# Kernel tuning notes

Hardware: AMD Instinct MI355X
Metric: run time of the kernel (lower is better)

Reference implementation:

```python
import jax, jax.numpy as jnp
import numpy as np

SIGMA = 0.5          # init kwarg sigma
PATCH = 5            # init kwarg patch_size
TILE = 32            # init kwarg patch_distance (tile side)
H_PARAM = (PATCH // 2) ** 0.5  # self.h = sqrt(patch_size//2)


def _nlm(tiles, sigma, p, Hp):
    # tiles: [b, c, h, w] -- faithful jax port of nlm()
    b, c, h, w = tiles.shape
    pad = p // 2
    padded = jnp.pad(tiles, ((0, 0), (0, 0), (pad, pad), (pad, pad)), mode='edge')  # replicate pad
    # unfold: all p*p shifted views -> [b, c, p*p, h, w] (channel-major then patch index,
    # matching torch unfold + unflatten(1, (c, p*p)))
    pats = jnp.stack([padded[:, :, i:i + h, j:j + w]
                      for i in range(p) for j in range(p)], axis=2)
    center = p * p // 2
    keep = np.array([k for k in range(p * p) if k != center])
    N = h * w
    d = c * (p * p - 1)
    yN = pats[:, :, keep].reshape(b, d, N).transpose(0, 2, 1)  # [b, N, d]
    # pairwise euclidean distance (cdist)
    sq = jnp.sum(yN * yN, axis=-1)  # [b, N]
    d2 = sq[:, :, None] + sq[:, None, :] - 2.0 * jnp.einsum('bnd,bmd->bnm', yN, yN)
    dist = jnp.sqrt(jnp.maximum(d2, 0.0))  # [b, N, N]
    density = jnp.exp(-dist / (2.0 * Hp ** 2 * sigma ** 2))
    # diag set to +inf in dist -> density diag = 0
    density = density * (1.0 - jnp.eye(N, dtype=density.dtype))
    weight = density / jnp.sum(density, axis=-1, keepdims=True)  # [b, N, N]
    y = tiles.reshape(b, c, N)  # [b, c, N]
    mmse = jnp.einsum('bnm,bcm->bcn', weight, y)  # weighted sum of pixel values
    return mmse.reshape(b, c, h, w)


def reference(image):
    # Tile image into non-overlapping TILE x TILE tiles, run nlm batched, fold back.
    b, c, h, w = image.shape
    T = TILE
    nh, nw = h // T, w // T
    tiles = image.reshape(b, c, nh, T, nw, T).transpose(0, 2, 4, 1, 3, 5)
    tiles = tiles.reshape(b * nh * nw, c, T, T)
    out = _nlm(tiles, SIGMA, PATCH, H_PARAM)
    out = out.reshape(b, nh, nw, c, T, T).transpose(0, 3, 1, 4, 2, 5)
    return out.reshape(b, c, h, w)


def setup_inputs() -> dict:
    key = jax.random.key(0)
    image = jax.random.uniform(key, (1, 3, 320, 320), dtype=jnp.float32)
    return {"image": image}
```

## Files before the change

kernel.cpp:

```cpp
#include <hip/hip_runtime.h>
#include <math.h>

#define TS   32
#define PT   36
#define NPIX 1024
#define DF   72
#define KP   96
#define IMH  320
#define IMW  320
#define NTW  10
#define NTILE 100

#define F_UNITS_PER_TILE 12288
#define FHI_BYTES (NTILE * F_UNITS_PER_TILE * 16)
#define SQ_OFF    (2 * FHI_BYTES)

#define K2LOG2E 2.0813689810056077f

typedef __attribute__((ext_vector_type(8))) short bf16x8;
typedef __attribute__((ext_vector_type(8))) unsigned short u16x8;
typedef __attribute__((ext_vector_type(4))) float f32x4;
typedef __attribute__((ext_vector_type(4))) __fp16 f16x4;
typedef __attribute__((ext_vector_type(2))) __fp16 f16x2;

__global__ __launch_bounds__(256)
void nlm_feat_kernel(const float* __restrict__ img,
                     u16x8* __restrict__ Fhi, float* __restrict__ Sq)
{
    __shared__ float Ploc[3][6][36];
    __shared__ int   ofsl[KP];
    const int tid  = threadIdx.x;
    const int part = blockIdx.x;
    const int tile = blockIdx.y;
    const int by   = (tile / NTW) * TS;
    const int bx   = (tile % NTW) * TS;
    const float* Pf = &Ploc[0][0][0];

    for (int idx = tid; idx < 3 * 6 * 36; idx += 256) {
        int c   = idx / 216;
        int rem = idx - c * 216;
        int yl  = rem / 36;
        int x   = rem - yl * 36;
        int y   = 2 * part + yl;
        int iy  = min(max(y - 2, 0), TS - 1);
        int ix  = min(max(x - 2, 0), TS - 1);
        Ploc[c][yl][x] = img[(c * IMH + by + iy) * IMW + bx + ix];
    }
    if (tid < KP) {
        int k = tid, v = 0;
        if (k < DF) {
            int c = k / 24, o = k - c * 24;
            int kk = o + (o >= 12);
            int i = kk / 5, j = kk - (kk / 5) * 5;
            v = c * 216 + i * 36 + j;
        }
        ofsl[k] = v;
    }
    __syncthreads();

    if (tid < 64) {
        int m  = part * 64 + tid;
        int my = m >> 5, mx = m & 31;
        int ly0 = my - 2 * part;
        float s = 0.f;
        #pragma unroll
        for (int k = 0; k < 25; ++k) {
            if (k == 12) continue;
            int i = k / 5, j = k - (k / 5) * 5;
            float v0 = Ploc[0][ly0 + i][mx + j];
            float v1 = Ploc[1][ly0 + i][mx + j];
            float v2 = Ploc[2][ly0 + i][mx + j];
            s = fmaf(v0, v0, s); s = fmaf(v1, v1, s); s = fmaf(v2, v2, s);
        }
        Sq[tile * NPIX + m] = s * K2LOG2E;
    }

    #pragma unroll
    for (int q = 0; q < 3; ++q) {
        int u    = part * 768 + q * 256 + tid;
        int row  = u & 15;
        int c4   = (u >> 4) & 3;
        int rks  = u >> 6;
        int ks   = rks - (rks / 3) * 3;
        int rt   = rks / 3;
        int r    = rt * 16 + row;
        int lbase = ((r >> 5) - 2 * part) * 36 + (r & 31);
        u16x8 h;
        #pragma unroll
        for (int j = 0; j < 8; ++j) {
            int k = ks * 32 + c4 * 8 + j;
            unsigned short hs = 0;
            if (k < DF) {
                float f = Pf[lbase + ofsl[k]];
                unsigned int uu = __float_as_uint(f);
                hs = (unsigned short)((uu + 0x7fffu + ((uu >> 16) & 1u)) >> 16);
            }
            h[j] = hs;
        }
        Fhi[tile * F_UNITS_PER_TILE + u] = h;
    }
}

__global__ __launch_bounds__(512)
__attribute__((amdgpu_waves_per_eu(4, 8)))
void nlm_gemm_kernel(const float* __restrict__ img,
                     const bf16x8* __restrict__ Fhi,
                     const float* __restrict__ SqK, float* __restrict__ out)
{
    __shared__ __fp16 Yhi[4][1032];
    __shared__ __fp16 Ylo[4][1032];
    __shared__ float red[8][2][16][4];

    const int tid  = threadIdx.x;
    const int lane = tid & 63;
    const int wv   = tid >> 6;
    const int i0   = blockIdx.x;
    const int w    = (i0 & 7) * 400 + (i0 >> 3);
    const int tile = w >> 5;
    const int rtA  = (w & 31) * 2;
    const int by   = (tile / NTW) * TS;
    const int bx   = (tile % NTW) * TS;
    const int quad = lane >> 4;
    const int col  = lane & 15;
    const int ycol = col & 3;

    const bf16x8* FHt = Fhi + tile * F_UNITS_PER_TILE;
    const float*  Sqt = SqK + tile * NPIX;

    for (int idx = tid; idx < 1024; idx += 512) {
        int c = idx >> 8, m4 = (idx & 255) << 2;
        f32x4 v = {1.f, 1.f, 1.f, 1.f};
        if (c < 3) v = *(const f32x4*)&img[(c * IMH + by + (m4 >> 5)) * IMW + bx + (m4 & 31)];
        f16x4 h, l;
        #pragma unroll
        for (int j = 0; j < 4; ++j) {
            h[j] = (__fp16)v[j];
            l[j] = (__fp16)(v[j] - (float)h[j]);
        }
        *(f16x4*)&Yhi[c][m4] = h;
        *(f16x4*)&Ylo[c][m4] = l;
    }

    bf16x8 bN[2][3];
    #pragma unroll
    for (int t = 0; t < 2; ++t)
        #pragma unroll
        for (int ks = 0; ks < 3; ++ks)
            bN[t][ks] = FHt[((rtA + t) * 3 + ks) * 64 + lane];
    asm volatile(""
        : "+v"(bN[0][0]), "+v"(bN[0][1]), "+v"(bN[0][2]),
          "+v"(bN[1][0]), "+v"(bN[1][1]), "+v"(bN[1][2]));

    float snK[2];
    #pragma unroll
    for (int t = 0; t < 2; ++t)
        snK[t] = Sqt[(rtA + t) * 16 + col];

    f32x4 DpvH0 = {0.f, 0.f, 0.f, 0.f};
    f32x4 DpvL0 = {0.f, 0.f, 0.f, 0.f};
    f32x4 DpvH1 = {0.f, 0.f, 0.f, 0.f};
    f32x4 DpvL1 = {0.f, 0.f, 0.f, 0.f};

    __syncthreads();

    const int mtBase = wv * 8;

    bf16x8 aS[3][3];
    f32x4  sqS[3];
    f16x4  bhS[3], blS[3];

#define LOADF(mt_, si)                                          \
    do {                                                        \
        int _mt = (mt_);                                        \
        aS[si][0] = FHt[(_mt * 3 + 0) * 64 + lane];             \
        aS[si][1] = FHt[(_mt * 3 + 1) * 64 + lane];             \
        aS[si][2] = FHt[(_mt * 3 + 2) * 64 + lane];             \
        sqS[si] = *(const f32x4*)&Sqt[_mt * 16 + quad * 4];     \
        bhS[si] = *(const f16x4*)&Yhi[ycol][_mt * 16 + quad * 4]; \
        blS[si] = *(const f16x4*)&Ylo[ycol][_mt * 16 + quad * 4]; \
    } while (0)

#define COMPUTE(mt_, si)                                                             \
    do {                                                                             \
        int _mt = (mt_);                                                             \
        f32x4 C0 = {0.f, 0.f, 0.f, 0.f};                                             \
        f32x4 C1 = {0.f, 0.f, 0.f, 0.f};                                             \
        C0 = __builtin_amdgcn_mfma_f32_16x16x32_bf16(aS[si][0], bN[0][0], C0, 0, 0, 0); \
        C1 = __builtin_amdgcn_mfma_f32_16x16x32_bf16(aS[si][0], bN[1][0], C1, 0, 0, 0); \
        C0 = __builtin_amdgcn_mfma_f32_16x16x32_bf16(aS[si][1], bN[0][1], C0, 0, 0, 0); \
        C1 = __builtin_amdgcn_mfma_f32_16x16x32_bf16(aS[si][1], bN[1][1], C1, 0, 0, 0); \
        C0 = __builtin_amdgcn_mfma_f32_16x16x32_bf16(aS[si][2], bN[0][2], C0, 0, 0, 0); \
        C1 = __builtin_amdgcn_mfma_f32_16x16x32_bf16(aS[si][2], bN[1][2], C1, 0, 0, 0); \
        _Pragma("unroll")                                                            \
        for (int t = 0; t < 2; ++t) {                                                \
            f32x4 C = t ? C1 : C0;                                                   \
            float d[4];                                                              \
            _Pragma("unroll")                                                        \
            for (int i = 0; i < 4; ++i) {                                            \
                float s2 = fmaxf(fmaf(-2.0f * K2LOG2E, C[i], sqS[si][i] + snK[t]), 0.f); \
                d[i] = __builtin_amdgcn_exp2f(-__builtin_amdgcn_sqrtf(s2));          \
            }                                                                        \
            if (_mt == rtA + t) {                                                    \
                _Pragma("unroll")                                                    \
                for (int i = 0; i < 4; ++i)                                          \
                    if (quad * 4 + i == col) d[i] = 0.f;                             \
            }                                                                        \
            f16x2 p0 = __builtin_amdgcn_cvt_pkrtz(d[0], d[1]);                       \
            f16x2 p1 = __builtin_amdgcn_cvt_pkrtz(d[2], d[3]);                       \
            f16x4 wp = __builtin_shufflevector(p0, p1, 0, 1, 2, 3);                  \
            if (t == 0) {                                                            \
                DpvH0 = __builtin_amdgcn_mfma_f32_16x16x16f16(wp, bhS[si], DpvH0, 0, 0, 0); \
                DpvL0 = __builtin_amdgcn_mfma_f32_16x16x16f16(wp, blS[si], DpvL0, 0, 0, 0); \
            } else {                                                                 \
                DpvH1 = __builtin_amdgcn_mfma_f32_16x16x16f16(wp, bhS[si], DpvH1, 0, 0, 0); \
                DpvL1 = __builtin_amdgcn_mfma_f32_16x16x16f16(wp, blS[si], DpvL1, 0, 0, 0); \
            }                                                                        \
        }                                                                            \
    } while (0)

    LOADF(mtBase + 0, 0);
    LOADF(mtBase + 1, 1);
    #pragma unroll
    for (int it = 0; it < 8; ++it) {
        if (it + 2 < 8) LOADF(mtBase + it + 2, (it + 2) % 3);
        COMPUTE(mtBase + it, it % 3);
    }
#undef LOADF
#undef COMPUTE

    if (col < 4) {
        #pragma unroll
        for (int i = 0; i < 4; ++i) {
            red[wv][0][quad * 4 + i][col] = DpvH0[i] + DpvL0[i];
            red[wv][1][quad * 4 + i][col] = DpvH1[i] + DpvL1[i];
        }
    }
    __syncthreads();

    if (tid < 128) {
        int n = tid >> 2, c = tid & 3;
        int t = n >> 4, r = n & 15;
        float s = 0.f;
        #pragma unroll
        for (int ww = 0; ww < 8; ++ww)
            s += red[ww][t][r][c];
        float rs = __shfl(s, (tid & 63) | 3, 64);
        if (c < 3) {
            int nn = rtA * 16 + n;
            int gy = by + (nn >> 5), gx = bx + (nn & 31);
            out[(c * IMH + gy) * IMW + gx] = s * (1.0f / rs);
        }
    }
}

extern "C" void kernel_launch(void* const* d_in, const int* in_sizes, int n_in,
                              void* d_out, int out_size, void* d_ws, size_t ws_size,
                              hipStream_t stream) {
    const float* img = (const float*)d_in[0];
    float* out = (float*)d_out;
    char* ws = (char*)d_ws;
    u16x8* Fhi = (u16x8*)ws;
    float* Sq  = (float*)(ws + SQ_OFF);

    dim3 fgrid(16, NTILE);
    nlm_feat_kernel<<<fgrid, 256, 0, stream>>>(img, Fhi, Sq);
    nlm_gemm_kernel<<<dim3(3200), 512, 0, stream>>>(img, (const bf16x8*)Fhi, Sq, out);
}
```

Measured before the change: 114.0 us.

## Fold squared-norm bias into MFMA accumulator and replace exp/sqrt with LDS table

```diff
diff --git a/kernel.cpp b/kernel.cpp
--- a/kernel.cpp
+++ b/kernel.cpp
@@ -16,10 +16,12 @@
 #define SQ_OFF    (2 * FHI_BYTES)
 
 #define K2LOG2E 2.0813689810056077f
+#define FSCALE  2.0402789f
 
 typedef __attribute__((ext_vector_type(8))) short bf16x8;
 typedef __attribute__((ext_vector_type(8))) unsigned short u16x8;
 typedef __attribute__((ext_vector_type(4))) float f32x4;
+typedef __attribute__((ext_vector_type(2))) float f32x2;
 typedef __attribute__((ext_vector_type(4))) __fp16 f16x4;
 typedef __attribute__((ext_vector_type(2))) __fp16 f16x2;
 
@@ -91,7 +93,7 @@
             int k = ks * 32 + c4 * 8 + j;
             unsigned short hs = 0;
             if (k < DF) {
-                float f = Pf[lbase + ofsl[k]];
+                float f = Pf[lbase + ofsl[k]] * FSCALE;
                 unsigned int uu = __float_as_uint(f);
                 hs = (unsigned short)((uu + 0x7fffu + ((uu >> 16) & 1u)) >> 16);
             }
@@ -110,6 +112,7 @@
     __shared__ __fp16 Yhi[4][1032];
     __shared__ __fp16 Ylo[4][1032];
     __shared__ float red[8][2][16][4];
+    __shared__ f32x2 Tbl[704];
 
     const int tid  = threadIdx.x;
     const int lane = tid & 63;
@@ -127,6 +130,15 @@
     const bf16x8* FHt = Fhi + tile * F_UNITS_PER_TILE;
     const float*  Sqt = SqK + tile * NPIX;
 
+    for (int idx = tid; idx < 704; idx += 512) {
+        unsigned blo = (unsigned)(idx + 3648) << 18;
+        float xlo = __uint_as_float(blo);
+        float xhi = __uint_as_float(blo + 262144u);
+        float flo = __builtin_amdgcn_exp2f(-__builtin_amdgcn_sqrtf(xlo));
+        float fhi = __builtin_amdgcn_exp2f(-__builtin_amdgcn_sqrtf(xhi));
+        Tbl[idx] = (f32x2){flo, fhi - flo};
+    }
+
     for (int idx = tid; idx < 1024; idx += 512) {
         int c = idx >> 8, m4 = (idx & 255) << 2;
         f32x4 v = {1.f, 1.f, 1.f, 1.f};
@@ -142,11 +154,14 @@
     }
 
     bf16x8 bN[2][3];
+    bf16x8 sgn;
+    #pragma unroll
+    for (int j = 0; j < 8; ++j) sgn[j] = (short)0x8000;
     #pragma unroll
     for (int t = 0; t < 2; ++t)
         #pragma unroll
         for (int ks = 0; ks < 3; ++ks)
-            bN[t][ks] = FHt[((rtA + t) * 3 + ks) * 64 + lane];
+            bN[t][ks] = FHt[((rtA + t) * 3 + ks) * 64 + lane] ^ sgn;
     asm volatile(""
         : "+v"(bN[0][0]), "+v"(bN[0][1]), "+v"(bN[0][2]),
           "+v"(bN[1][0]), "+v"(bN[1][1]), "+v"(bN[1][2]));
@@ -183,8 +198,10 @@
 #define COMPUTE(mt_, si)                                                             \
     do {                                                                             \
         int _mt = (mt_);                                                             \
-        f32x4 C0 = {0.f, 0.f, 0.f, 0.f};                                             \
-        f32x4 C1 = {0.f, 0.f, 0.f, 0.f};                                             \
+        f32x4 C0 = {sqS[si][0] + snK[0], sqS[si][1] + snK[0],                        \
+                    sqS[si][2] + snK[0], sqS[si][3] + snK[0]};                       \
+        f32x4 C1 = {sqS[si][0] + snK[1], sqS[si][1] + snK[1],                        \
+                    sqS[si][2] + snK[1], sqS[si][3] + snK[1]};                       \
         C0 = __builtin_amdgcn_mfma_f32_16x16x32_bf16(aS[si][0], bN[0][0], C0, 0, 0, 0); \
         C1 = __builtin_amdgcn_mfma_f32_16x16x32_bf16(aS[si][0], bN[1][0], C1, 0, 0, 0); \
         C0 = __builtin_amdgcn_mfma_f32_16x16x32_bf16(aS[si][1], bN[0][1], C0, 0, 0, 0); \
@@ -197,8 +214,12 @@
             float d[4];                                                              \
             _Pragma("unroll")                                                        \
             for (int i = 0; i < 4; ++i) {                                            \
-                float s2 = fmaxf(fmaf(-2.0f * K2LOG2E, C[i], sqS[si][i] + snK[t]), 0.f); \
-                d[i] = __builtin_amdgcn_exp2f(-__builtin_amdgcn_sqrtf(s2));          \
+                float s2 = fmaxf(C[i], 1.220703125e-4f);               \
+                unsigned b = __float_as_uint(s2);                                    \
+                int idx = (int)(b >> 18) - 3648;                     \
+                float fr = (float)(b & 0x3ffffu) * 3.814697265625e-06f;              \
+                f32x2 te = Tbl[idx];                                                 \
+                d[i] = fmaf(te[1], fr, te[0]);                                       \
             }                                                                        \
             if (_mt == rtA + t) {                                                    \
                 _Pragma("unroll")                                                    \
```

Result: slower. 121.8 us (+6.8%).
